# Kernel tuning notes

Measured on AMD Instinct MI355X. Metric: run time of the kernel, lower is better.

The kernel has to match this reference:

```python
import jax, jax.numpy as jnp
import numpy as np

NUM_CLASSES = 10
OUT_DIM = 16
NUM_ROUTING = 3
ROUTING_BIAS = 0.1


def _squash(s):
    # s: [B, C, D]; norm over last (out_capsule) dim, matches torch norm(dim=2)
    norm = jnp.linalg.norm(s, axis=2, keepdims=True)
    # s / (1+norm^2) / norm * norm^2 == s * norm / (1 + norm^2)
    return s * norm / (1.0 + norm * norm)


def setup_inputs() -> dict:
    key = jax.random.key(0)
    k1, k2 = jax.random.split(key)
    B, N, IN_DIM = 256, 2304, 8
    x = jax.random.normal(k1, (B, N, IN_DIM), dtype=jnp.float32)
    # kaiming-normal-ish init for W [N, in_dim, classes*out_dim]
    W = jax.random.normal(k2, (N, IN_DIM, NUM_CLASSES * OUT_DIM), dtype=jnp.float32) * np.sqrt(2.0 / IN_DIM)
    return {"x": x, "W": W}


def reference(x, W):
    B, N, _ = x.shape
    # broadcast-multiply+sum in original == per-capsule matmul
    u_hat = jnp.einsum('bni,nio->bno', x, W).reshape(B, N, NUM_CLASSES, OUT_DIM)
    u_hat_sg = jax.lax.stop_gradient(u_hat)
    b = jnp.zeros((B, N, NUM_CLASSES), dtype=x.dtype)
    v = None
    for i in range(NUM_ROUTING):
        c = jax.nn.softmax(b, axis=2)  # [B, N, C]
        if i == NUM_ROUTING - 1:
            s = jnp.einsum('bnc,bncd->bcd', c, u_hat) + ROUTING_BIAS
            v = _squash(s)
        else:
            s = jnp.einsum('bnc,bncd->bcd', c, u_hat_sg) + ROUTING_BIAS
            # NOTE: original updates b with pre-squash s (not v) -- kept faithful
            b = b + jnp.einsum('bncd,bcd->bnc', u_hat_sg, s)
    return v
```

## Files before the change

### kernel.cpp

```cpp
#include <hip/hip_runtime.h>
#include <math.h>

#define B_TOT   256
#define N_TOT   2304
#define IN_DIM  8
#define NC      10
#define OD      16
#define CD      160
#define RBIAS   0.1f

#define BTILE    64
#define NS       128
#define NPB      (N_TOT / NS)
#define NTHREADS 640
#define XR       (NPB * IN_DIM + 4)
#define LB       72
#define NF4      (B_TOT * CD / 4)

#define NXCD     8

#define RCOLS    8
#define RGRPS    32
#define RYPER    (NS / RGRPS)

template <int FIRST>
__global__ __launch_bounds__(NTHREADS) void routing_round(
    const float* __restrict__ x,
    const float* __restrict__ W,
    const float* __restrict__ S_acc,
    float* __restrict__ part)
{
    __shared__ float sh_x[BTILE * XR];
    __shared__ float sh_lg[2][NC * LB];

    const int tid = threadIdx.x;

    const int o      = blockIdx.x;
    const int xcd    = o & (NXCD - 1);
    const int r      = o >> 3;
    const int cuslot = r & 31;
    const int pairid = r >> 5;
    const int ySlab  = xcd * 16 + (cuslot & 15);
    const int b0     = ((cuslot >> 4) * 2 + pairid) * BTILE;
    const int n0     = ySlab * NPB;

    const int b   = tid & 63;
    const int cu  = __builtin_amdgcn_readfirstlane(tid >> 6);

    {
        const int XT4 = BTILE * (NPB * IN_DIM / 4);
        for (int k = tid; k < XT4; k += NTHREADS) {
            int bb   = k / (NPB * 2);
            int off4 = k - bb * (NPB * 2);
            float4 v = *(const float4*)(x + ((size_t)(b0 + bb) * N_TOT + n0) * IN_DIM + off4 * 4);
            *(float4*)(&sh_x[bb * XR + off4 * 4]) = v;
        }
    }

    float S[OD];
    if (!FIRST) {
        const float4* sp = (const float4*)(S_acc + (size_t)(b0 + b) * CD + cu * OD);
        #pragma unroll
        for (int q = 0; q < 4; q++) ((float4*)S)[q] = sp[q];
    }

    float acc[OD];
    #pragma unroll
    for (int d = 0; d < OD; d++) acc[d] = 0.f;

    __syncthreads();

    const float* Wc = W + cu * OD;

    for (int nn = 0; nn < NPB; nn++) {
        float xf[IN_DIM];
        {
            const float4* xp = (const float4*)(&sh_x[b * XR + nn * IN_DIM]);
            ((float4*)xf)[0] = xp[0];
            ((float4*)xf)[1] = xp[1];
        }

        const float* Wn = Wc + (size_t)(n0 + nn) * (IN_DIM * CD);
        float u[OD];
        #pragma unroll
        for (int d = 0; d < OD; d++) u[d] = xf[0] * Wn[d];
        #pragma unroll
        for (int i = 1; i < IN_DIM; i++) {
            const float* Wi = Wn + i * CD;
            #pragma unroll
            for (int d = 0; d < OD; d++) u[d] = fmaf(xf[i], Wi[d], u[d]);
        }

        if (!FIRST) {
            const int cur = nn & 1;
            float lg = 0.f;
            #pragma unroll
            for (int d = 0; d < OD; d++) lg = fmaf(u[d], S[d], lg);
            sh_lg[cur][cu * LB + b] = lg;
            __syncthreads();

            float m = -1e30f;
            float row[NC];
            #pragma unroll
            for (int k = 0; k < NC; k++) {
                row[k] = sh_lg[cur][k * LB + b];
                m = fmaxf(m, row[k]);
            }
            float den = 0.f;
            #pragma unroll
            for (int k = 0; k < NC; k++) den += __expf(row[k] - m);
            float cw = __expf(lg - m) / den;

            #pragma unroll
            for (int d = 0; d < OD; d++) acc[d] = fmaf(cw, u[d], acc[d]);
        } else {
            #pragma unroll
            for (int d = 0; d < OD; d++) acc[d] += u[d];
        }
    }

    float* dst = part + ((size_t)ySlab * B_TOT + (b0 + b)) * CD + cu * OD;
    #pragma unroll
    for (int q = 0; q < 4; q++)
        ((float4*)dst)[q] = ((float4*)acc)[q];
}

__global__ __launch_bounds__(256) void reduce_round(
    const float* __restrict__ part,
    float* __restrict__ S_acc,
    float* __restrict__ v_out,
    float scale, int round)
{
    __shared__ float4 sh[RGRPS][RCOLS];

    const int col = threadIdx.x & (RCOLS - 1);
    const int grp = threadIdx.x >> 3;
    const int g   = blockIdx.x * RCOLS + col;

    const float4* p4 = (const float4*)part + (size_t)grp * NF4 + g;
    float4 s = { 0.f, 0.f, 0.f, 0.f };
    #pragma unroll
    for (int y = 0; y < RYPER; y++) {
        float4 t = p4[(size_t)y * RGRPS * NF4];
        s.x += t.x; s.y += t.y; s.z += t.z; s.w += t.w;
    }
    sh[grp][col] = s;
    __syncthreads();

    if (threadIdx.x < RCOLS) {
        float4 t = { 0.f, 0.f, 0.f, 0.f };
        #pragma unroll
        for (int k = 0; k < RGRPS; k++) {
            float4 q = sh[k][col];
            t.x += q.x; t.y += q.y; t.z += q.z; t.w += q.w;
        }
        t.x = t.x * scale + RBIAS;
        t.y = t.y * scale + RBIAS;
        t.z = t.z * scale + RBIAS;
        t.w = t.w * scale + RBIAS;

        if (round == 0) {
            ((float4*)S_acc)[g] = t;
        } else if (round == 1) {
            float4 o = ((float4*)S_acc)[g];
            o.x += t.x; o.y += t.y; o.z += t.z; o.w += t.w;
            ((float4*)S_acc)[g] = o;
        } else {
            float ss = t.x * t.x + t.y * t.y + t.z * t.z + t.w * t.w;
            ss += __shfl_xor(ss, 1, 64);
            ss += __shfl_xor(ss, 2, 64);
            float norm = sqrtf(ss);
            float k2 = norm / (1.0f + ss);
            float4 v = { t.x * k2, t.y * k2, t.z * k2, t.w * k2 };
            ((float4*)v_out)[g] = v;
        }
    }
}

extern "C" void kernel_launch(void* const* d_in, const int* in_sizes, int n_in,
                              void* d_out, int out_size, void* d_ws, size_t ws_size,
                              hipStream_t stream) {
    const float* x = (const float*)d_in[0];
    const float* W = (const float*)d_in[1];
    float* out = (float*)d_out;

    float* part  = (float*)d_ws;
    float* S_acc = part + (size_t)NS * B_TOT * CD;

    const dim3 rgrid(NS * (B_TOT / BTILE));
    const int  RG = NF4 / RCOLS;

    routing_round<1><<<rgrid, NTHREADS, 0, stream>>>(x, W, S_acc, part);
    reduce_round<<<RG, 256, 0, stream>>>(part, S_acc, out, 0.1f, 0);

    routing_round<0><<<rgrid, NTHREADS, 0, stream>>>(x, W, S_acc, part);
    reduce_round<<<RG, 256, 0, stream>>>(part, S_acc, out, 1.0f, 1);

    routing_round<0><<<rgrid, NTHREADS, 0, stream>>>(x, W, S_acc, part);
    reduce_round<<<RG, 256, 0, stream>>>(part, S_acc, out, 1.0f, 2);
}
```

Before: 197.1 us.

## Stage per-capsule W rows in LDS via double-buffered global_load_lds

Measured after the change: 212.7 us. 7.9% more time.

```diff
diff --git a/kernel.cpp b/kernel.cpp
--- a/kernel.cpp
+++ b/kernel.cpp
@@ -16,6 +16,7 @@
 #define XR       (NPB * IN_DIM + 4)
 #define LB       72
 #define NF4      (B_TOT * CD / 4)
+#define WROW     (IN_DIM * CD)
 
 #define NXCD     8
 
@@ -23,14 +24,19 @@
 #define RGRPS    32
 #define RYPER    (NS / RGRPS)
 
+#define GLDS16(gp, lp) __builtin_amdgcn_global_load_lds(                 \
+    (const __attribute__((address_space(1))) void*)(gp),                  \
+    (__attribute__((address_space(3))) void*)(lp), 16, 0, 0)
+
 template <int FIRST>
-__global__ __launch_bounds__(NTHREADS) void routing_round(
+__global__ __launch_bounds__(NTHREADS, 5) void routing_round(
     const float* __restrict__ x,
     const float* __restrict__ W,
     const float* __restrict__ S_acc,
     float* __restrict__ part)
 {
-    __shared__ float sh_x[BTILE * XR];
+    __shared__ __align__(16) float sh_x[BTILE * XR];
+    __shared__ __align__(16) float sh_w[2][WROW];
     __shared__ float sh_lg[2][NC * LB];
 
     const int tid = threadIdx.x;
@@ -47,6 +53,9 @@
     const int b   = tid & 63;
     const int cu  = __builtin_amdgcn_readfirstlane(tid >> 6);
 
+    if (cu < 5)
+        GLDS16(W + (size_t)n0 * WROW + cu * 256 + b * 4, &sh_w[0][cu * 256]);
+
     {
         const int XT4 = BTILE * (NPB * IN_DIM / 4);
         for (int k = tid; k < XT4; k += NTHREADS) {
@@ -68,11 +77,16 @@
     #pragma unroll
     for (int d = 0; d < OD; d++) acc[d] = 0.f;
 
+    asm volatile("s_waitcnt vmcnt(0)" ::: "memory");
     __syncthreads();
 
-    const float* Wc = W + cu * OD;
-
     for (int nn = 0; nn < NPB; nn++) {
+        const int cur = nn & 1;
+
+        if (cu < 5 && nn + 1 < NPB)
+            GLDS16(W + (size_t)(n0 + nn + 1) * WROW + cu * 256 + b * 4,
+                   &sh_w[cur ^ 1][cu * 256]);
+
         float xf[IN_DIM];
         {
             const float4* xp = (const float4*)(&sh_x[b * XR + nn * IN_DIM]);
@@ -80,23 +94,31 @@
             ((float4*)xf)[1] = xp[1];
         }
 
-        const float* Wn = Wc + (size_t)(n0 + nn) * (IN_DIM * CD);
+        const float* wb = &sh_w[cur][cu * OD];
         float u[OD];
         #pragma unroll
-        for (int d = 0; d < OD; d++) u[d] = xf[0] * Wn[d];
-        #pragma unroll
-        for (int i = 1; i < IN_DIM; i++) {
-            const float* Wi = Wn + i * CD;
-            #pragma unroll
-            for (int d = 0; d < OD; d++) u[d] = fmaf(xf[i], Wi[d], u[d]);
+        for (int d = 0; d < OD; d++) u[d] = 0.f;
+        #pragma unroll
+        for (int i = 0; i < IN_DIM; i++) {
+            const float4* wp = (const float4*)(wb + i * CD);
+            const float4 wa = wp[0], wbv = wp[1], wcv = wp[2], wdv = wp[3];
+            const float xi = xf[i];
+            u[0]  = fmaf(xi, wa.x,  u[0]);  u[1]  = fmaf(xi, wa.y,  u[1]);
+            u[2]  = fmaf(xi, wa.z,  u[2]);  u[3]  = fmaf(xi, wa.w,  u[3]);
+            u[4]  = fmaf(xi, wbv.x, u[4]);  u[5]  = fmaf(xi, wbv.y, u[5]);
+            u[6]  = fmaf(xi, wbv.z, u[6]);  u[7]  = fmaf(xi, wbv.w, u[7]);
+            u[8]  = fmaf(xi, wcv.x, u[8]);  u[9]  = fmaf(xi, wcv.y, u[9]);
+            u[10] = fmaf(xi, wcv.z, u[10]); u[11] = fmaf(xi, wcv.w, u[11]);
+            u[12] = fmaf(xi, wdv.x, u[12]); u[13] = fmaf(xi, wdv.y, u[13]);
+            u[14] = fmaf(xi, wdv.z, u[14]); u[15] = fmaf(xi, wdv.w, u[15]);
         }
 
         if (!FIRST) {
-            const int cur = nn & 1;
             float lg = 0.f;
             #pragma unroll
             for (int d = 0; d < OD; d++) lg = fmaf(u[d], S[d], lg);
             sh_lg[cur][cu * LB + b] = lg;
+            asm volatile("s_waitcnt vmcnt(0)" ::: "memory");
             __syncthreads();
 
             float m = -1e30f;
@@ -116,6 +138,10 @@
         } else {
             #pragma unroll
             for (int d = 0; d < OD; d++) acc[d] += u[d];
+            if (nn + 1 < NPB) {
+                asm volatile("s_waitcnt vmcnt(0)" ::: "memory");
+                __syncthreads();
+            }
         }
     }
 
```

## Replace partial-sum buffer and reduction pass with atomic accumulation into transposed raws

Applied to the files above, without the earlier changes.

Measured after the change: 202.1 us. 1.03x slower.

```diff
diff --git a/kernel.cpp b/kernel.cpp
--- a/kernel.cpp
+++ b/kernel.cpp
@@ -15,20 +15,17 @@
 #define NTHREADS 640
 #define XR       (NPB * IN_DIM + 4)
 #define LB       72
-#define NF4      (B_TOT * CD / 4)
+#define WROW     (IN_DIM * CD)
+#define SRAW     (B_TOT * CD)
 
 #define NXCD     8
-
-#define RCOLS    8
-#define RGRPS    32
-#define RYPER    (NS / RGRPS)
 
 template <int FIRST>
 __global__ __launch_bounds__(NTHREADS) void routing_round(
     const float* __restrict__ x,
     const float* __restrict__ W,
     const float* __restrict__ S_acc,
-    float* __restrict__ part)
+    float* __restrict__ rawT)
 {
     __shared__ float sh_x[BTILE * XR];
     __shared__ float sh_lg[2][NC * LB];
@@ -80,7 +77,7 @@
             ((float4*)xf)[1] = xp[1];
         }
 
-        const float* Wn = Wc + (size_t)(n0 + nn) * (IN_DIM * CD);
+        const float* Wn = Wc + (size_t)(n0 + nn) * WROW;
         float u[OD];
         #pragma unroll
         for (int d = 0; d < OD; d++) u[d] = xf[0] * Wn[d];
@@ -119,61 +116,52 @@
         }
     }
 
-    float* dst = part + ((size_t)ySlab * B_TOT + (b0 + b)) * CD + cu * OD;
+    float* dst = rawT + b0 + b;
     #pragma unroll
-    for (int q = 0; q < 4; q++)
-        ((float4*)dst)[q] = ((float4*)acc)[q];
+    for (int d = 0; d < OD; d++)
+        atomicAdd(dst + (size_t)(cu * OD + d) * B_TOT, acc[d]);
 }
 
-__global__ __launch_bounds__(256) void reduce_round(
-    const float* __restrict__ part,
+__global__ __launch_bounds__(256) void zero_raws(float4* __restrict__ p)
+{
+    p[(size_t)blockIdx.x * 256 + threadIdx.x] = (float4){0.f, 0.f, 0.f, 0.f};
+}
+
+__global__ __launch_bounds__(256) void finalize_round(
+    const float* __restrict__ rawT,
     float* __restrict__ S_acc,
     float* __restrict__ v_out,
-    float scale, int round)
+    int mode)
 {
-    __shared__ float4 sh[RGRPS][RCOLS];
+    const int p   = blockIdx.x * 256 + threadIdx.x;
+    const int b   = p / 40;
+    const int rem = p - b * 40;
+    const int cd0 = rem * 4;
 
-    const int col = threadIdx.x & (RCOLS - 1);
-    const int grp = threadIdx.x >> 3;
-    const int g   = blockIdx.x * RCOLS + col;
+    float t0 = rawT[(size_t)(cd0 + 0) * B_TOT + b];
+    float t1 = rawT[(size_t)(cd0 + 1) * B_TOT + b];
+    float t2 = rawT[(size_t)(cd0 + 2) * B_TOT + b];
+    float t3 = rawT[(size_t)(cd0 + 3) * B_TOT + b];
 
-    const float4* p4 = (const float4*)part + (size_t)grp * NF4 + g;
-    float4 s = { 0.f, 0.f, 0.f, 0.f };
-    #pragma unroll
-    for (int y = 0; y < RYPER; y++) {
-        float4 t = p4[(size_t)y * RGRPS * NF4];
-        s.x += t.x; s.y += t.y; s.z += t.z; s.w += t.w;
-    }
-    sh[grp][col] = s;
-    __syncthreads();
-
-    if (threadIdx.x < RCOLS) {
-        float4 t = { 0.f, 0.f, 0.f, 0.f };
-        #pragma unroll
-        for (int k = 0; k < RGRPS; k++) {
-            float4 q = sh[k][col];
-            t.x += q.x; t.y += q.y; t.z += q.z; t.w += q.w;
-        }
-        t.x = t.x * scale + RBIAS;
-        t.y = t.y * scale + RBIAS;
-        t.z = t.z * scale + RBIAS;
-        t.w = t.w * scale + RBIAS;
-
-        if (round == 0) {
-            ((float4*)S_acc)[g] = t;
-        } else if (round == 1) {
-            float4 o = ((float4*)S_acc)[g];
-            o.x += t.x; o.y += t.y; o.z += t.z; o.w += t.w;
-            ((float4*)S_acc)[g] = o;
-        } else {
-            float ss = t.x * t.x + t.y * t.y + t.z * t.z + t.w * t.w;
-            ss += __shfl_xor(ss, 1, 64);
-            ss += __shfl_xor(ss, 2, 64);
-            float norm = sqrtf(ss);
-            float k2 = norm / (1.0f + ss);
-            float4 v = { t.x * k2, t.y * k2, t.z * k2, t.w * k2 };
-            ((float4*)v_out)[g] = v;
-        }
+    if (mode == 0) {
+        float4 o = { t0 * 0.1f + RBIAS, t1 * 0.1f + RBIAS,
+                     t2 * 0.1f + RBIAS, t3 * 0.1f + RBIAS };
+        ((float4*)S_acc)[p] = o;
+    } else if (mode == 1) {
+        float4 o = ((const float4*)S_acc)[p];
+        o.x += t0 + RBIAS; o.y += t1 + RBIAS;
+        o.z += t2 + RBIAS; o.w += t3 + RBIAS;
+        ((float4*)S_acc)[p] = o;
+    } else {
+        const float s0 = t0 + RBIAS, s1 = t1 + RBIAS;
+        const float s2 = t2 + RBIAS, s3 = t3 + RBIAS;
+        float ss = s0 * s0 + s1 * s1 + s2 * s2 + s3 * s3;
+        ss += __shfl_xor(ss, 1, 64);
+        ss += __shfl_xor(ss, 2, 64);
+        const float norm = sqrtf(ss);
+        const float k2 = norm / (1.0f + ss);
+        float4 v = { s0 * k2, s1 * k2, s2 * k2, s3 * k2 };
+        ((float4*)v_out)[p] = v;
     }
 }
 
@@ -184,18 +172,21 @@
     const float* W = (const float*)d_in[1];
     float* out = (float*)d_out;
 
-    float* part  = (float*)d_ws;
-    float* S_acc = part + (size_t)NS * B_TOT * CD;
+    float* raw0  = (float*)d_ws;
+    float* raw1  = raw0 + SRAW;
+    float* raw2  = raw1 + SRAW;
+    float* S_acc = raw2 + SRAW;
 
-    const dim3 rgrid(NS * (B_TOT / BTILE));
-    const int  RG = NF4 / RCOLS;
+    const dim3 rgrid(512);
 
-    routing_round<1><<<rgrid, NTHREADS, 0, stream>>>(x, W, S_acc, part);
-    reduce_round<<<RG, 256, 0, stream>>>(part, S_acc, out, 0.1f, 0);
+    zero_raws<<<120, 256, 0, stream>>>((float4*)raw0);
 
-    routing_round<0><<<rgrid, NTHREADS, 0, stream>>>(x, W, S_acc, part);
-    reduce_round<<<RG, 256, 0, stream>>>(part, S_acc, out, 1.0f, 1);
+    routing_round<1><<<rgrid, NTHREADS, 0, stream>>>(x, W, S_acc, raw0);
+    finalize_round<<<40, 256, 0, stream>>>(raw0, S_acc, out, 0);
 
-    routing_round<0><<<rgrid, NTHREADS, 0, stream>>>(x, W, S_acc, part);
-    reduce_round<<<RG, 256, 0, stream>>>(part, S_acc, out, 1.0f, 2);
+    routing_round<0><<<rgrid, NTHREADS, 0, stream>>>(x, W, S_acc, raw1);
+    finalize_round<<<40, 256, 0, stream>>>(raw1, S_acc, out, 1);
+
+    routing_round<0><<<rgrid, NTHREADS, 0, stream>>>(x, W, S_acc, raw2);
+    finalize_round<<<40, 256, 0, stream>>>(raw2, S_acc, out, 2);
 }
```
